# Kernel tuning notes

Measured on AMD Instinct MI355X. Metric: run time of the kernel, lower is better.

## Reference

```python
import jax, jax.numpy as jnp
import numpy as np

B, T, H = 32, 500, 1612            # 6 regions * 256 + iti 76
ALM_EXC_LO, ALM_EXC_HI = 1280, 1460  # alm starts at 5*256; exc = 0.7*256 = 180 units
T_CONST = 0.1


def _base_firing():
    # per-region base firing rates: str 0, gpe 0.8, stn 0.5, snr 0.8, thal 0.8, alm 0, iti 0
    sizes = [256, 256, 256, 256, 256, 256, 76]
    rates = [0.0, 0.8, 0.5, 0.8, 0.8, 0.0, 0.0]
    return jnp.asarray(np.concatenate([np.full(s, r, np.float32) for s, r in zip(sizes, rates)]))


def setup_inputs() -> dict:
    key = jax.random.key(0)
    ks = jax.random.split(key, 12)
    inp = jax.random.normal(ks[0], (B, T, 1), jnp.float32)
    cue_inp = jax.random.normal(ks[1], (B, T, 1), jnp.float32)
    hn = jax.random.uniform(ks[2], (1, B, H), jnp.float32)
    xn = 0.1 * jax.random.normal(ks[3], (1, B, H), jnp.float32)
    inhib_stim = 0.01 * jax.random.normal(ks[4], (B, T, H), jnp.float32)
    W_rec = jax.random.uniform(ks[5], (H, H), jnp.float32, 0.0, 0.01)
    # binary connectivity mask (stands in for the sparse/cell-type block masks)
    W_rec_mask = (jax.random.uniform(ks[6], (H, H), jnp.float32) < 0.5).astype(jnp.float32)
    W_rec_fixed = jnp.zeros((H, H), jnp.float32)
    # diagonal +/-1 sign matrix (Dale's law), kept as a full matrix as in the source
    signs = jnp.where(jax.random.uniform(ks[7], (H,), jnp.float32) < 0.5, -1.0, 1.0)
    W_rec_sign = jnp.diag(signs)
    W_inp = jax.random.uniform(ks[8], (H, 1), jnp.float32, 0.0, 0.01)
    W_cue = jax.random.uniform(ks[9], (H, 1), jnp.float32, 0.0, 0.01)
    out_weight_alm = (1.0 / 256.0) * jnp.ones((1, ALM_EXC_HI - ALM_EXC_LO), jnp.float32)
    base_firing = _base_firing()
    return {"inp": inp, "cue_inp": cue_inp, "hn": hn, "xn": xn, "inhib_stim": inhib_stim,
            "W_rec": W_rec, "W_rec_mask": W_rec_mask, "W_rec_fixed": W_rec_fixed,
            "W_rec_sign": W_rec_sign, "W_inp": W_inp, "W_cue": W_cue,
            "out_weight_alm": out_weight_alm, "base_firing": base_firing}


def reference(inp, cue_inp, hn, xn, inhib_stim, W_rec, W_rec_mask, W_rec_fixed,
              W_rec_sign, W_inp, W_cue, out_weight_alm, base_firing):
    # Dale's-law constrained effective recurrent weights:
    # (mask * hardtanh(W, 0, 1) + fixed) @ sign
    W_eff = (W_rec_mask * jnp.clip(W_rec, 0.0, 1.0) + W_rec_fixed) @ W_rec_sign  # [H,H]
    x0 = xn[0]  # [B,H]
    h0 = hn[0]  # [B,H]

    def step(carry, ts):
        x, h = carry
        i_t, c_t, s_t = ts  # [B,1],[B,1],[B,H]
        ff = h @ W_eff.T + i_t @ W_inp.T + c_t @ W_cue.T + s_t
        x_new = x + T_CONST * (-x + ff)
        h_new = jax.nn.relu(x_new + base_firing)
        return (x_new, h_new), h_new

    ts = (jnp.transpose(inp, (1, 0, 2)), jnp.transpose(cue_inp, (1, 0, 2)),
          jnp.transpose(inhib_stim, (1, 0, 2)))
    _, hs = jax.lax.scan(step, (x0, h0), ts)  # hs: [T,B,H]
    out = hs[:, :, ALM_EXC_LO:ALM_EXC_HI] @ out_weight_alm.T  # [T,B,out_dim]
    return jnp.transpose(out, (1, 0, 2))  # [B,T,out_dim]
```

## Files before the change

### kernel.cpp

```cpp
#include <hip/hip_runtime.h>

#define BB 32
#define TT 500
#define HH 1612
#define HP 1664
#define HR 1624
#define NW 8
#define THREADS 512
#define NWG 256
#define RPW 8
#define KPW (HP / NW)
#define ALO 1280
#define AHI 1460
#define WSTR 1668
#define RSTR 36
#define T_CONST 0.1f

__global__ void init_kernel(const float* __restrict__ hn, const float* __restrict__ xn,
                            const float* __restrict__ Wsign, float* __restrict__ out,
                            float* __restrict__ hA, float* __restrict__ xs,
                            float* __restrict__ sdiag)
{
    const int gid = blockIdx.x * blockDim.x + threadIdx.x;
    const int gsz = gridDim.x * blockDim.x;
    for (int i = gid; i < HP; i += gsz)
        sdiag[i] = (i < HH) ? Wsign[(size_t)i * HH + i] : 0.f;
    for (int i = gid; i < HP * BB; i += gsz) {
        const int k = i >> 5, b = i & 31;
        hA[(k >> 2) * (BB * 4) + b * 4 + (k & 3)] = (k < HH) ? hn[b * HH + k] : 0.f;
    }
    for (int i = gid; i < HH * BB; i += gsz) {
        const int j = i >> 5, b = i & 31;
        xs[i] = xn[b * HH + j];
    }
    for (int i = gid; i < BB * TT; i += gsz) out[i] = 0.f;
}

__global__ void weff_kernel(const float* __restrict__ Wrec, const float* __restrict__ Wmask,
                            const float* __restrict__ Wfix, const float* __restrict__ sdiag,
                            float* __restrict__ Weff)
{
    const int gid = blockIdx.x * blockDim.x + threadIdx.x;
    const int gsz = gridDim.x * blockDim.x;
    const int nq = HR * (HP / 4);
    for (int qi = gid; qi < nq; qi += gsz) {
        const int j = qi / (HP / 4);
        const int k = (qi % (HP / 4)) * 4;
        float4 v = make_float4(0.f, 0.f, 0.f, 0.f);
        if (j < HH && k < HH) {
            const float4 w = *(const float4*)&Wrec[(size_t)j * HH + k];
            const float4 m = *(const float4*)&Wmask[(size_t)j * HH + k];
            const float4 f = *(const float4*)&Wfix[(size_t)j * HH + k];
            const float4 s = *(const float4*)&sdiag[k];
            v.x = (m.x * fminf(fmaxf(w.x, 0.f), 1.f) + f.x) * s.x;
            v.y = (m.y * fminf(fmaxf(w.y, 0.f), 1.f) + f.y) * s.y;
            v.z = (m.z * fminf(fmaxf(w.z, 0.f), 1.f) + f.z) * s.z;
            v.w = (m.w * fminf(fmaxf(w.w, 0.f), 1.f) + f.w) * s.w;
        }
        *(float4*)&Weff[(size_t)j * HP + k] = v;
    }
}

template <bool PRE>
__global__ __launch_bounds__(THREADS, 1) void step_kernel(
    const int t,
    const float* __restrict__ hc,  float* __restrict__ hnx,
    float* __restrict__ xs,        const float* __restrict__ Weff,
    const float* __restrict__ Wrec,const float* __restrict__ Wmask,
    const float* __restrict__ Wfix,const float* __restrict__ sdiag,
    const float* __restrict__ inp, const float* __restrict__ cue,
    const float* __restrict__ stim,const float* __restrict__ Winp,
    const float* __restrict__ Wcue,const float* __restrict__ walm,
    const float* __restrict__ base,float* __restrict__ out)
{
    __shared__ float Wlds[RPW * WSTR];
    __shared__ float red[NW * RPW * RSTR];
    __shared__ float almb[RPW * RSTR];

    const int tid  = threadIdx.x;
    const int wg   = blockIdx.x;
    const int wave = tid >> 6;
    const int lane = tid & 63;
    const int bl   = lane & 15;
    const int rq   = (lane >> 4) & 3;

    const int r0    = (wg * HH) / NWG;
    const int r1    = ((wg + 1) * HH) / NWG;
    const int nreal = r1 - r0;

    const int er = tid & 7, eb = tid >> 3;
    const int ej = r0 + er;
    const bool eactive = (tid < 256) && (er < nreal);
    float sv = 0.f, iv = 0.f, cv = 0.f, xv = 0.f;
    float basej = 0.f, winpj = 0.f, wcuej = 0.f, walmj = 0.f;
    if (eactive) {
        sv    = __builtin_nontemporal_load(
                    &stim[(size_t)eb * (TT * HH) + (size_t)t * HH + ej]);
        iv    = inp[eb * TT + t];
        cv    = cue[eb * TT + t];
        xv    = xs[ej * BB + eb];
        basej = base[ej];
        winpj = Winp[ej];
        wcuej = Wcue[ej];
        walmj = (ej >= ALO && ej < AHI) ? walm[ej - ALO] : 0.f;
    }
    const bool has_alm = (r1 > ALO) && (r0 < AHI);

    if constexpr (PRE) {
        for (int i = tid; i < RPW * (HP / 4); i += THREADS) {
            const int r = i / (HP / 4), k = (i % (HP / 4)) * 4;
            const float4 v = *(const float4*)&Weff[(size_t)(r0 + r) * HP + k];
            *(float4*)&Wlds[r * WSTR + k] = v;
        }
    } else {
        for (int i = tid; i < RPW * (HP / 4); i += THREADS) {
            const int r = i / (HP / 4), k = (i % (HP / 4)) * 4;
            const int j = r0 + r;
            float4 v = make_float4(0.f, 0.f, 0.f, 0.f);
            if (r < nreal && k < HH) {
                const float4 w = *(const float4*)&Wrec[(size_t)j * HH + k];
                const float4 m = *(const float4*)&Wmask[(size_t)j * HH + k];
                const float4 f = *(const float4*)&Wfix[(size_t)j * HH + k];
                const float4 s = *(const float4*)&sdiag[k];
                v.x = (m.x * fminf(fmaxf(w.x, 0.f), 1.f) + f.x) * s.x;
                v.y = (m.y * fminf(fmaxf(w.y, 0.f), 1.f) + f.y) * s.y;
                v.z = (m.z * fminf(fmaxf(w.z, 0.f), 1.f) + f.z) * s.z;
                v.w = (m.w * fminf(fmaxf(w.w, 0.f), 1.f) + f.w) * s.w;
            }
            *(float4*)&Wlds[r * WSTR + k] = v;
        }
    }
    __syncthreads();

    float a00 = 0.f, a01 = 0.f, a10 = 0.f, a11 = 0.f;
    {
        const int kbase = wave * KPW;
        const float* __restrict__ hq  = hc + kbase * BB + bl * 4;
        const float* __restrict__ w0p = &Wlds[rq * WSTR + kbase];
        const float* __restrict__ w1p = w0p + 4 * WSTR;
        #pragma unroll 4
        for (int q = 0; q < KPW / 4; ++q) {
            const float4 h0 = *(const float4*)(hq + q * 128);
            const float4 h1 = *(const float4*)(hq + q * 128 + 64);
            const float4 w0 = *(const float4*)(w0p + q * 4);
            const float4 w1 = *(const float4*)(w1p + q * 4);
            a00 = fmaf(w0.x, h0.x, a00); a00 = fmaf(w0.y, h0.y, a00);
            a00 = fmaf(w0.z, h0.z, a00); a00 = fmaf(w0.w, h0.w, a00);
            a01 = fmaf(w0.x, h1.x, a01); a01 = fmaf(w0.y, h1.y, a01);
            a01 = fmaf(w0.z, h1.z, a01); a01 = fmaf(w0.w, h1.w, a01);
            a10 = fmaf(w1.x, h0.x, a10); a10 = fmaf(w1.y, h0.y, a10);
            a10 = fmaf(w1.z, h0.z, a10); a10 = fmaf(w1.w, h0.w, a10);
            a11 = fmaf(w1.x, h1.x, a11); a11 = fmaf(w1.y, h1.y, a11);
            a11 = fmaf(w1.z, h1.z, a11); a11 = fmaf(w1.w, h1.w, a11);
        }
    }

    red[(wave * RPW + rq    ) * RSTR + bl     ] = a00;
    red[(wave * RPW + rq    ) * RSTR + bl + 16] = a01;
    red[(wave * RPW + rq + 4) * RSTR + bl     ] = a10;
    red[(wave * RPW + rq + 4) * RSTR + bl + 16] = a11;
    __syncthreads();

    float av = 0.f;
    if (tid < 256) {
        float ff = 0.f;
        #pragma unroll
        for (int w2 = 0; w2 < NW; ++w2)
            ff += red[(w2 * RPW + er) * RSTR + eb];
        if (eactive) {
            ff += sv;
            ff = fmaf(iv, winpj, ff);
            ff = fmaf(cv, wcuej, ff);
            xv = fmaf(T_CONST, ff - xv, xv);
            xs[ej * BB + eb] = xv;
            const float hval = fmaxf(xv + basej, 0.f);
            hnx[(ej >> 2) * (BB * 4) + eb * 4 + (ej & 3)] = hval;
            av = hval * walmj;
        }
    }

    if (has_alm) {
        if (tid < 256) almb[er * RSTR + eb] = av;
        __syncthreads();
        if (tid < 32) {
            float s8 = 0.f;
            #pragma unroll
            for (int r = 0; r < RPW; ++r) s8 += almb[r * RSTR + tid];
            atomicAdd(&out[tid * TT + t], s8);
        }
    }
}

extern "C" void kernel_launch(void* const* d_in, const int* in_sizes, int n_in,
                              void* d_out, int out_size, void* d_ws, size_t ws_size,
                              hipStream_t stream) {
    const float* inp   = (const float*)d_in[0];
    const float* cue   = (const float*)d_in[1];
    const float* hn    = (const float*)d_in[2];
    const float* xn    = (const float*)d_in[3];
    const float* stim  = (const float*)d_in[4];
    const float* Wrec  = (const float*)d_in[5];
    const float* Wmask = (const float*)d_in[6];
    const float* Wfix  = (const float*)d_in[7];
    const float* Wsign = (const float*)d_in[8];
    const float* Winp  = (const float*)d_in[9];
    const float* Wcue  = (const float*)d_in[10];
    const float* walm  = (const float*)d_in[11];
    const float* base  = (const float*)d_in[12];
    float* out = (float*)d_out;

    const size_t weff_elems = (size_t)HR * HP;
    const size_t need = (weff_elems + 3 * (size_t)HP * BB + HP) * sizeof(float);
    const bool pre = (ws_size >= need);

    float* Weff, *hA, *hB, *xs, *sdiag;
    if (pre) {
        Weff  = (float*)d_ws;
        hA    = Weff + weff_elems;
    } else {
        Weff  = nullptr;
        hA    = (float*)d_ws;
    }
    hB    = hA + (size_t)HP * BB;
    xs    = hB + (size_t)HP * BB;
    sdiag = xs + (size_t)HP * BB;

    init_kernel<<<NWG, 256, 0, stream>>>(hn, xn, Wsign, out, hA, xs, sdiag);
    if (pre)
        weff_kernel<<<NWG, 256, 0, stream>>>(Wrec, Wmask, Wfix, sdiag, Weff);

    float* hc = hA;
    float* hx = hB;
    for (int t = 0; t < TT; ++t) {
        if (pre)
            step_kernel<true><<<NWG, THREADS, 0, stream>>>(
                t, hc, hx, xs, Weff, nullptr, nullptr, nullptr, nullptr,
                inp, cue, stim, Winp, Wcue, walm, base, out);
        else
            step_kernel<false><<<NWG, THREADS, 0, stream>>>(
                t, hc, hx, xs, nullptr, Wrec, Wmask, Wfix, sdiag,
                inp, cue, stim, Winp, Wcue, walm, base, out);
        float* tmp = hc; hc = hx; hx = tmp;
    }
}
```

Before: 5.447 ms.

## Add persistent cooperative kernel with W_eff in LDS and grid-wide counter barrier

```diff
diff --git a/kernel.cpp b/kernel.cpp
--- a/kernel.cpp
+++ b/kernel.cpp
@@ -14,7 +14,182 @@
 #define AHI 1460
 #define WSTR 1668
 #define RSTR 36
+#define HBUF (HP * BB)
 #define T_CONST 0.1f
+
+
+__global__ void pers_init(const float* __restrict__ hn, const float* __restrict__ Wsign,
+                          float* __restrict__ out, float* __restrict__ hbase,
+                          float* __restrict__ sdiag, unsigned* __restrict__ cnt)
+{
+    const int gid = blockIdx.x * blockDim.x + threadIdx.x;
+    const int gsz = gridDim.x * blockDim.x;
+    for (int i = gid; i < HP; i += gsz)
+        sdiag[i] = (i < HH) ? Wsign[(size_t)i * HH + i] : 0.f;
+    for (int i = gid; i < HP * BB; i += gsz) {
+        const int k = i >> 5, b = i & 31;
+        hbase[(k >> 2) * 128 + b * 4 + (k & 3)] = (k < HH) ? hn[b * HH + k] : 0.f;
+    }
+    for (int i = gid; i < TT * 13 * 128; i += gsz) {
+        const int buf = 1 + i / (13 * 128);
+        const int off = i % (13 * 128);
+        hbase[(size_t)buf * HBUF + 403 * 128 + off] = 0.f;
+    }
+    for (int i = gid; i < BB * TT; i += gsz) out[i] = 0.f;
+    for (int i = gid; i < 512; i += gsz) cnt[i] = 0u;
+}
+
+__global__ __launch_bounds__(THREADS, 1) void pers_kernel(
+    const float* __restrict__ xn,
+    const float* __restrict__ Wrec, const float* __restrict__ Wmask,
+    const float* __restrict__ Wfix, const float* __restrict__ sdiag,
+    const float* __restrict__ inp,  const float* __restrict__ cue,
+    const float* __restrict__ stim, const float* __restrict__ Winp,
+    const float* __restrict__ Wcue, const float* __restrict__ walm,
+    const float* __restrict__ base, float* __restrict__ out,
+    float* __restrict__ hbase,      unsigned* __restrict__ cnt)
+{
+    __shared__ float Wlds[RPW * WSTR];
+    __shared__ float red[NW * RPW * RSTR];
+    __shared__ float almb[RPW * RSTR];
+
+    const int tid  = threadIdx.x;
+    const int wg   = blockIdx.x;
+    const int wave = tid >> 6;
+    const int lane = tid & 63;
+    const int bl   = lane & 15;
+    const int rq   = (lane >> 4) & 3;
+
+    const int r0    = (wg * HH) / NWG;
+    const int r1    = ((wg + 1) * HH) / NWG;
+    const int nreal = r1 - r0;
+
+    for (int i = tid; i < RPW * (HP / 4); i += THREADS) {
+        const int r = i / (HP / 4), k = (i % (HP / 4)) * 4;
+        const int j = r0 + r;
+        float4 v = make_float4(0.f, 0.f, 0.f, 0.f);
+        if (r < nreal && k < HH) {
+            const float4 w = *(const float4*)&Wrec[(size_t)j * HH + k];
+            const float4 m = *(const float4*)&Wmask[(size_t)j * HH + k];
+            const float4 f = *(const float4*)&Wfix[(size_t)j * HH + k];
+            const float4 s = *(const float4*)&sdiag[k];
+            v.x = (m.x * fminf(fmaxf(w.x, 0.f), 1.f) + f.x) * s.x;
+            v.y = (m.y * fminf(fmaxf(w.y, 0.f), 1.f) + f.y) * s.y;
+            v.z = (m.z * fminf(fmaxf(w.z, 0.f), 1.f) + f.z) * s.z;
+            v.w = (m.w * fminf(fmaxf(w.w, 0.f), 1.f) + f.w) * s.w;
+        }
+        *(float4*)&Wlds[r * WSTR + k] = v;
+    }
+
+    const int er = tid & 7, eb = tid >> 3;
+    const int ej = r0 + er;
+    const bool eactive = (tid < 256) && (er < nreal);
+    float xv = 0.f, basej = 0.f, winpj = 0.f, wcuej = 0.f, walmj = 0.f;
+    if (eactive) {
+        xv    = xn[eb * HH + ej];
+        basej = base[ej];
+        winpj = Winp[ej];
+        wcuej = Wcue[ej];
+        walmj = (ej >= ALO && ej < AHI) ? walm[ej - ALO] : 0.f;
+    }
+    const bool has_alm = (r1 > ALO) && (r0 < AHI);
+    const int kbase = wave * KPW;
+
+    __syncthreads();
+
+    for (int t = 0; t < TT; ++t) {
+        const float* __restrict__ hc = hbase + (size_t)t * HBUF;
+        float* __restrict__ hx       = hbase + (size_t)(t + 1) * HBUF;
+
+        float sv = 0.f, iv = 0.f, cv = 0.f;
+        if (eactive) {
+            sv = __builtin_nontemporal_load(
+                     &stim[(size_t)eb * (TT * HH) + (size_t)t * HH + ej]);
+            iv = inp[eb * TT + t];
+            cv = cue[eb * TT + t];
+        }
+
+        float a00 = 0.f, a01 = 0.f, a10 = 0.f, a11 = 0.f;
+        {
+            const float* __restrict__ hq  = hc + kbase * BB + bl * 4;
+            const float* __restrict__ w0p = &Wlds[rq * WSTR + kbase];
+            const float* __restrict__ w1p = w0p + 4 * WSTR;
+            #pragma unroll 4
+            for (int q = 0; q < KPW / 4; ++q) {
+                const float4 h0 = *(const float4*)(hq + q * 128);
+                const float4 h1 = *(const float4*)(hq + q * 128 + 64);
+                const float4 w0 = *(const float4*)(w0p + q * 4);
+                const float4 w1 = *(const float4*)(w1p + q * 4);
+                a00 = fmaf(w0.x, h0.x, a00); a00 = fmaf(w0.y, h0.y, a00);
+                a00 = fmaf(w0.z, h0.z, a00); a00 = fmaf(w0.w, h0.w, a00);
+                a01 = fmaf(w0.x, h1.x, a01); a01 = fmaf(w0.y, h1.y, a01);
+                a01 = fmaf(w0.z, h1.z, a01); a01 = fmaf(w0.w, h1.w, a01);
+                a10 = fmaf(w1.x, h0.x, a10); a10 = fmaf(w1.y, h0.y, a10);
+                a10 = fmaf(w1.z, h0.z, a10); a10 = fmaf(w1.w, h0.w, a10);
+                a11 = fmaf(w1.x, h1.x, a11); a11 = fmaf(w1.y, h1.y, a11);
+                a11 = fmaf(w1.z, h1.z, a11); a11 = fmaf(w1.w, h1.w, a11);
+            }
+        }
+
+        red[(wave * RPW + rq    ) * RSTR + bl     ] = a00;
+        red[(wave * RPW + rq    ) * RSTR + bl + 16] = a01;
+        red[(wave * RPW + rq + 4) * RSTR + bl     ] = a10;
+        red[(wave * RPW + rq + 4) * RSTR + bl + 16] = a11;
+        __syncthreads();
+
+        float av = 0.f;
+        if (tid < 256) {
+            float ff = 0.f;
+            #pragma unroll
+            for (int w2 = 0; w2 < NW; ++w2)
+                ff += red[(w2 * RPW + er) * RSTR + eb];
+            if (eactive) {
+                ff += sv;
+                ff = fmaf(iv, winpj, ff);
+                ff = fmaf(cv, wcuej, ff);
+                xv = fmaf(T_CONST, ff - xv, xv);
+                const float hval = fmaxf(xv + basej, 0.f);
+                __hip_atomic_store(&hx[(ej >> 2) * 128 + eb * 4 + (ej & 3)], hval,
+                                   __ATOMIC_RELAXED, __HIP_MEMORY_SCOPE_AGENT);
+                av = hval * walmj;
+            }
+        }
+
+        if (has_alm) {
+            if (tid < 256) almb[er * RSTR + eb] = av;
+            __syncthreads();
+            if (tid < 32) {
+                float s8 = 0.f;
+                #pragma unroll
+                for (int r = 0; r < RPW; ++r) s8 += almb[r * RSTR + tid];
+                atomicAdd(&out[tid * TT + t], s8);
+            }
+        }
+
+        if (t != TT - 1) {
+            __syncthreads();
+            if (tid == 0)
+                __hip_atomic_fetch_add(&cnt[(wg & 7) << 6], 1u,
+                                       __ATOMIC_RELAXED, __HIP_MEMORY_SCOPE_AGENT);
+            if (wave == 0) {
+                const unsigned target = 256u * (unsigned)(t + 1);
+                unsigned s;
+                do {
+                    unsigned v = (lane < 8)
+                        ? __hip_atomic_load(&cnt[lane << 6], __ATOMIC_RELAXED,
+                                            __HIP_MEMORY_SCOPE_AGENT)
+                        : 0u;
+                    v += __shfl_xor(v, 1);
+                    v += __shfl_xor(v, 2);
+                    v += __shfl_xor(v, 4);
+                    s = __shfl(v, 0);
+                } while (s < target);
+            }
+            __syncthreads();
+        }
+    }
+}
+
 
 __global__ void init_kernel(const float* __restrict__ hn, const float* __restrict__ xn,
                             const float* __restrict__ Wsign, float* __restrict__ out,
@@ -209,6 +384,23 @@
     const float* base  = (const float*)d_in[12];
     float* out = (float*)d_out;
 
+    const size_t pers_need = ((size_t)(TT + 1) * HBUF + HP) * sizeof(float) + 2048;
+    if (ws_size >= pers_need) {
+        float* hbase    = (float*)d_ws;
+        float* sdiag    = hbase + (size_t)(TT + 1) * HBUF;
+        unsigned* cnt   = (unsigned*)(sdiag + HP);
+
+        pers_init<<<NWG, 256, 0, stream>>>(hn, Wsign, out, hbase, sdiag, cnt);
+
+        void* args[] = { (void*)&xn, (void*)&Wrec, (void*)&Wmask, (void*)&Wfix,
+                         (void*)&sdiag, (void*)&inp, (void*)&cue, (void*)&stim,
+                         (void*)&Winp, (void*)&Wcue, (void*)&walm, (void*)&base,
+                         (void*)&out, (void*)&hbase, (void*)&cnt };
+        hipLaunchCooperativeKernel(reinterpret_cast<void*>(pers_kernel),
+                                   dim3(NWG), dim3(THREADS), args, 0, stream);
+        return;
+    }
+
     const size_t weff_elems = (size_t)HR * HP;
     const size_t need = (weff_elems + 3 * (size_t)HP * BB + HP) * sizeof(float);
     const bool pre = (ws_size >= need);
```

Result: faster. 5.139 ms (-5.7%).
